# Kernel tuning notes

Hardware: AMD Instinct MI355X
Metric: run time of the kernel (lower is better)

The kernel has to match this reference:

```python
import jax, jax.numpy as jnp
import numpy as np

B, Q, K, C, H, DH, OUT = 32, 512, 512, 256, 8, 32, 256


def setup_inputs() -> dict:
    key = jax.random.key(0)
    ks = jax.random.split(key, 11)
    s = 1.0 / np.sqrt(C)
    return {
        "q_data": jax.random.normal(ks[0], (B, Q, C), jnp.float32),
        "m_data": jax.random.normal(ks[1], (B, K, C), jnp.float32),
        "bias": jax.random.normal(ks[2], (B, 1, Q, K), jnp.float32),
        "nonbatched_bias": jax.random.normal(ks[3], (H, Q, K), jnp.float32),
        "query_w": jax.random.normal(ks[4], (C, H, DH), jnp.float32) * s,
        "key_w": jax.random.normal(ks[5], (C, H, DH), jnp.float32) * s,
        "value_w": jax.random.normal(ks[6], (C, H, DH), jnp.float32) * s,
        "gating_w": jax.random.normal(ks[7], (C, H, DH), jnp.float32) * s,
        "gating_b": jax.random.normal(ks[8], (H, DH), jnp.float32),
        "output_w": jax.random.normal(ks[9], (H, DH, OUT), jnp.float32) * (1.0 / np.sqrt(H * DH)),
        "output_b": jax.random.normal(ks[10], (OUT,), jnp.float32),
    }


def reference(q_data, m_data, bias, nonbatched_bias, query_w, key_w, value_w,
              gating_w, gating_b, output_w, output_b):
    key_dim = query_w.shape[-1]  # per-head key dim
    q = jnp.einsum('bqa,ahc->bqhc', q_data, query_w) * key_dim ** (-0.5)
    k = jnp.einsum('bka,ahc->bkhc', m_data, key_w)
    v = jnp.einsum('bka,ahc->bkhc', m_data, value_w)
    logits = jnp.einsum('bqhc,bkhc->bhqk', q, k) + bias  # [B,H,Q,K]
    logits = logits + nonbatched_bias[None]  # broadcast over batch
    logits = jnp.clip(logits, -1e8, 1e8)
    weights = jax.nn.softmax(logits, axis=-1)
    weighted_avg = jnp.einsum('bhqk,bkhc->bqhc', weights, v)
    gate = jax.nn.sigmoid(jnp.einsum('bqc,chv->bqhv', q_data, gating_w) + gating_b)
    weighted_avg = weighted_avg * gate
    return jnp.einsum('bqhc,hco->bqo', weighted_avg, output_w) + output_b
```

## Files before the change

kernel.cpp:

```cpp
#include <hip/hip_runtime.h>

typedef unsigned short u16;
typedef __attribute__((ext_vector_type(4))) short short4v;
typedef __attribute__((ext_vector_type(8))) short bf16x8;
typedef __attribute__((ext_vector_type(4))) float f32x4;

union Pack8 { u16 h[8]; int4 v; bf16x8 b; };
union Frag8 { bf16x8 v8; short4v h4[2]; };

__device__ __forceinline__ f32x4 mfma16(bf16x8 a, bf16x8 b, f32x4 c) {
    return __builtin_amdgcn_mfma_f32_16x16x32_bf16(a, b, c, 0, 0, 0);
}

__device__ __forceinline__ float bf2f(u16 u) {
    unsigned int x = ((unsigned int)u) << 16;
    return __builtin_bit_cast(float, x);
}

__device__ __forceinline__ u16 f2bf(float f) {
    unsigned int u = __builtin_bit_cast(unsigned int, f);
    u += 0x7FFF + ((u >> 16) & 1);
    return (u16)(u >> 16);
}

__global__ __launch_bounds__(256) void prep_w2(
    const float* __restrict__ qw, const float* __restrict__ kw,
    const float* __restrict__ vw, const float* __restrict__ gw,
    const float* __restrict__ ow,
    u16* __restrict__ wtq, u16* __restrict__ wtm, u16* __restrict__ wto)
{
    const int which = blockIdx.z;
    const float* s = which == 0 ? qw : which == 1 ? kw : which == 2 ? vw
                   : which == 3 ? gw : ow;
    u16* d; int roff;
    if (which == 0)      { d = wtq; roff = 0; }
    else if (which == 3) { d = wtq; roff = 256; }
    else if (which == 1) { d = wtm; roff = 0; }
    else if (which == 2) { d = wtm; roff = 256; }
    else                 { d = wto; roff = 0; }

    const int n0 = blockIdx.x * 64;
    const int c0 = blockIdx.y * 64;

    __shared__ float T[64][68];
    const int rr = threadIdx.x >> 2;
    const int sg = threadIdx.x & 3;
    #pragma unroll
    for (int j = 0; j < 4; ++j) {
        float4 v = *(const float4*)(&s[(size_t)(c0 + rr) * 256 + n0 + sg * 16 + j * 4]);
        *(float4*)(&T[rr][sg * 16 + j * 4]) = v;
    }
    __syncthreads();
    #pragma unroll
    for (int j = 0; j < 4; ++j) {
        union { u16 h[4]; uint2 v; } p;
        #pragma unroll
        for (int e = 0; e < 4; ++e)
            p.h[e] = f2bf(T[sg * 16 + j * 4 + e][rr]);
        *(uint2*)(&d[(size_t)(roff + n0 + rr) * 256 + c0 + sg * 16 + j * 4]) = p.v;
    }
}

__global__ __launch_bounds__(256) void proj128(
    const float* __restrict__ q_data, const float* __restrict__ m_data,
    const u16* __restrict__ wtq, const u16* __restrict__ wtm,
    const float* __restrict__ gating_b,
    u16* __restrict__ qbuf, u16* __restrict__ kbuf,
    u16* __restrict__ vbuf, u16* __restrict__ gbuf)
{
    const int src = blockIdx.z;
    const float* X = src ? m_data : q_data;
    const u16* W = src ? wtm : wtq;

    const int m0 = blockIdx.x * 128;
    const int n0 = blockIdx.y * 128;

    __shared__ __align__(16) u16 SMEM[2][128][72];
    #define Xs (SMEM[0])
    #define Ws (SMEM[1])

    const int tid  = threadIdx.x;
    const int wave = tid >> 6;
    const int wm   = wave >> 1, wn = wave & 1;
    const int lane = tid & 63;
    const int l16  = lane & 15;
    const int quad = lane >> 4;

    const f32x4 kZero = {0.f, 0.f, 0.f, 0.f};
    f32x4 acc[4][4];
    #pragma unroll
    for (int i = 0; i < 4; ++i)
        #pragma unroll
        for (int j = 0; j < 4; ++j) acc[i][j] = kZero;

    const int r  = tid >> 1;
    const int cs = (tid & 1) * 32;

    for (int k0 = 0; k0 < 256; k0 += 64) {
        __syncthreads();
        #pragma unroll
        for (int i = 0; i < 4; ++i) {
            const float4* xp = (const float4*)(&X[(size_t)(m0 + r) * 256 + k0 + cs + i * 8]);
            float4 xa = xp[0], xb = xp[1];
            Pack8 pk;
            pk.h[0] = f2bf(xa.x); pk.h[1] = f2bf(xa.y);
            pk.h[2] = f2bf(xa.z); pk.h[3] = f2bf(xa.w);
            pk.h[4] = f2bf(xb.x); pk.h[5] = f2bf(xb.y);
            pk.h[6] = f2bf(xb.z); pk.h[7] = f2bf(xb.w);
            *(int4*)(&Xs[r][cs + i * 8]) = pk.v;
            *(int4*)(&Ws[r][cs + i * 8]) = *(const int4*)(&W[(size_t)(n0 + r) * 256 + k0 + cs + i * 8]);
        }
        __syncthreads();
        #pragma unroll
        for (int ks = 0; ks < 2; ++ks) {
            bf16x8 a[4], bb[4];
            #pragma unroll
            for (int mf = 0; mf < 4; ++mf)
                a[mf] = *(const bf16x8*)(&Xs[wm * 64 + mf * 16 + l16][ks * 32 + quad * 8]);
            #pragma unroll
            for (int nf = 0; nf < 4; ++nf)
                bb[nf] = *(const bf16x8*)(&Ws[wn * 64 + nf * 16 + l16][ks * 32 + quad * 8]);
            #pragma unroll
            for (int mf = 0; mf < 4; ++mf)
                #pragma unroll
                for (int nf = 0; nf < 4; ++nf)
                    acc[mf][nf] = mfma16(a[mf], bb[nf], acc[mf][nf]);
        }
    }

    const bool second = (n0 >= 256);
    const int b = m0 >> 9, qi0 = m0 & 511;

    __syncthreads();
    u16* T = &SMEM[0][0][0];

    if (src == 1 && second) {
        #pragma unroll
        for (int nf = 0; nf < 4; ++nf) {
            const int nl_ = wn * 64 + nf * 16 + l16;
            #pragma unroll
            for (int mf = 0; mf < 4; ++mf)
                #pragma unroll
                for (int rr = 0; rr < 4; ++rr) {
                    const int ml = wm * 64 + mf * 16 + quad * 4 + rr;
                    T[nl_ * 136 + ml] = f2bf(acc[mf][nf][rr]);
                }
        }
        __syncthreads();
        const int row = tid >> 1, half = tid & 1;
        const int nl = (n0 - 256) + row;
        const int h = nl >> 5, c = nl & 31;
        u16* dst = &vbuf[((size_t)(b * 8 + h) * 32 + c) * 512 + qi0 + half * 64];
        #pragma unroll
        for (int i = 0; i < 8; ++i)
            *(int4*)(&dst[i * 8]) = *(const int4*)(&T[row * 136 + half * 64 + i * 8]);
        return;
    }

    #pragma unroll
    for (int nf = 0; nf < 4; ++nf) {
        const int nl_ = wn * 64 + nf * 16 + l16;
        const int ng = n0 + nl_;
        #pragma unroll
        for (int mf = 0; mf < 4; ++mf) {
            #pragma unroll
            for (int rr = 0; rr < 4; ++rr) {
                const int ml = wm * 64 + mf * 16 + quad * 4 + rr;
                float v = acc[mf][nf][rr];
                u16 val;
                if (src == 0 && !second) {
                    val = f2bf(v * 0.17677669529663689f);
                } else if (src == 0) {
                    val = f2bf(1.0f / (1.0f + __expf(-(v + gating_b[ng - 256]))));
                } else {
                    val = f2bf(v);
                }
                T[ml * 136 + nl_] = val;
            }
        }
    }
    __syncthreads();

    if (src == 0 && second) {
        const int ml = tid >> 1, sub = tid & 1;
        u16* dst = &gbuf[(size_t)(m0 + ml) * 256 + (n0 - 256) + sub * 64];
        #pragma unroll
        for (int i = 0; i < 8; ++i)
            *(int4*)(&dst[i * 8]) = *(const int4*)(&T[ml * 136 + sub * 64 + i * 8]);
    } else {
        u16* D = (src == 0) ? qbuf : kbuf;
        const int hl = tid & 3, h0 = n0 >> 5;
        #pragma unroll
        for (int p = 0; p < 2; ++p) {
            const int ml = p * 64 + (tid >> 2);
            u16* dst = &D[((size_t)(b * 8 + h0 + hl) * 512 + qi0 + ml) * 32];
            #pragma unroll
            for (int i = 0; i < 4; ++i)
                *(int4*)(&dst[i * 8]) = *(const int4*)(&T[ml * 136 + hl * 32 + i * 8]);
        }
    }
    #undef Xs
    #undef Ws
}

__global__ __launch_bounds__(256) void attn_kernel(
    const u16* __restrict__ qbuf, const u16* __restrict__ kbuf,
    const u16* __restrict__ vbuf, const float* __restrict__ bias,
    const float* __restrict__ nb, const u16* __restrict__ gbuf,
    u16* __restrict__ waG)
{
    const int b = blockIdx.z, h = blockIdx.y, q0 = blockIdx.x * 64;
    const int tid  = threadIdx.x;
    const int wave = tid >> 6;
    const int lane = tid & 63;
    const int l16  = lane & 15;
    const int quad = lane >> 4;

    __shared__ __align__(16) u16   Ks[64][40];
    __shared__ __align__(16) u16   Vs[32][72];
    __shared__ __align__(16) float Bs[4][16][68];

    const int qrow_base = q0 + wave * 16;
    bf16x8 aQ = *(const bf16x8*)(&qbuf[((b * 8 + h) * 512 + qrow_base + l16) * 32 + quad * 8]);

    const f32x4 kZero = {0.f, 0.f, 0.f, 0.f};
    f32x4 oacc[2] = {kZero, kZero};
    float lsum = 0.f;

    const int krow = tid >> 2, kseg = tid & 3;
    const int vr = tid >> 3,  vseg = tid & 7;
    const int br = lane >> 2, bc = (lane & 3) * 16;
    const u16* kbase = &kbuf[(size_t)(b * 8 + h) * 512 * 32];
    const u16* vbase = &vbuf[(size_t)(b * 8 + h) * 32 * 512];
    const float* bl = &bias[((size_t)b * 512 + qrow_base + br) * 512];
    const float* nl = &nb[((size_t)h * 512 + qrow_base + br) * 512];

    int4 kreg = *(const int4*)(&kbase[krow * 32 + kseg * 8]);
    int4 vreg = *(const int4*)(&vbase[vr * 512 + vseg * 8]);
    float4 bbp[4], nnp[4];
    #pragma unroll
    for (int i = 0; i < 4; ++i) {
        bbp[i] = *(const float4*)(&bl[bc + i * 4]);
        nnp[i] = *(const float4*)(&nl[bc + i * 4]);
    }

    for (int kt = 0; kt < 8; ++kt) {
        __syncthreads();
        *(int4*)(&Ks[krow][kseg * 8]) = kreg;
        *(int4*)(&Vs[vr][vseg * 8])   = vreg;
        #pragma unroll
        for (int i = 0; i < 4; ++i) {
            float4 s = make_float4(bbp[i].x + nnp[i].x, bbp[i].y + nnp[i].y,
                                   bbp[i].z + nnp[i].z, bbp[i].w + nnp[i].w);
            *(float4*)(&Bs[wave][br][bc + i * 4]) = s;
        }
        __syncthreads();

        if (kt < 7) {
            const int kk1 = (kt + 1) * 64;
            kreg = *(const int4*)(&kbase[(kk1 + krow) * 32 + kseg * 8]);
            vreg = *(const int4*)(&vbase[vr * 512 + kk1 + vseg * 8]);
            #pragma unroll
            for (int i = 0; i < 4; ++i) {
                bbp[i] = *(const float4*)(&bl[kk1 + bc + i * 4]);
                nnp[i] = *(const float4*)(&nl[kk1 + bc + i * 4]);
            }
        }

        float p[4][4];
        #pragma unroll
        for (int kn = 0; kn < 4; ++kn) {
            f32x4 cb = *(const f32x4*)(&Bs[wave][l16][kn * 16 + quad * 4]);
            bf16x8 aK = *(const bf16x8*)(&Ks[kn * 16 + l16][quad * 8]);
            f32x4 st = mfma16(aK, aQ, cb);
            #pragma unroll
            for (int rr = 0; rr < 4; ++rr) {
                float pv = __expf(st[rr]);
                p[kn][rr] = pv;
                lsum += pv;
            }
        }

        #pragma unroll
        for (int pr = 0; pr < 2; ++pr) {
            Frag8 bP;
            #pragma unroll
            for (int rr = 0; rr < 4; ++rr) {
                bP.h4[0][rr] = (short)f2bf(p[2 * pr][rr]);
                bP.h4[1][rr] = (short)f2bf(p[2 * pr + 1][rr]);
            }
            #pragma unroll
            for (int ct = 0; ct < 2; ++ct) {
                Frag8 aV;
                aV.h4[0] = *(const short4v*)(&Vs[ct * 16 + l16][pr * 32 + quad * 4]);
                aV.h4[1] = *(const short4v*)(&Vs[ct * 16 + l16][pr * 32 + 16 + quad * 4]);
                oacc[ct] = mfma16(aV.v8, bP.v8, oacc[ct]);
            }
        }
    }

    lsum += __shfl_xor(lsum, 16, 64);
    lsum += __shfl_xor(lsum, 32, 64);
    const float linv = 1.0f / lsum;

    u16* OsW = (u16*)&Bs[wave][0][0];
    #pragma unroll
    for (int ct = 0; ct < 2; ++ct)
        #pragma unroll
        for (int rr = 0; rr < 4; ++rr)
            OsW[l16 * 40 + ct * 16 + quad * 4 + rr] = f2bf(oacc[ct][rr] * linv);

    __asm__ __volatile__("" ::: "memory");

    const int orow = lane >> 2, osg = lane & 3;
    Pack8 ov, gv;
    ov.v = *(const int4*)(&OsW[orow * 40 + osg * 8]);
    size_t gidx = ((size_t)(b * 512 + q0 + wave * 16 + orow)) * 256 + h * 32 + osg * 8;
    gv.v = *(const int4*)(&gbuf[gidx]);
    Pack8 outv;
    #pragma unroll
    for (int i = 0; i < 8; ++i)
        outv.h[i] = f2bf(bf2f(ov.h[i]) * bf2f(gv.h[i]));
    *(int4*)(&waG[gidx]) = outv.v;
}

__global__ __launch_bounds__(256) void out_gemm128(
    const u16* __restrict__ waG, const u16* __restrict__ wto,
    const float* __restrict__ out_b, float* __restrict__ out)
{
    const int m0 = blockIdx.x * 128;
    const int n0 = blockIdx.y * 128;

    __shared__ __align__(16) u16 Xs[128][72];
    __shared__ __align__(16) u16 Ws[128][72];

    const int tid  = threadIdx.x;
    const int wave = tid >> 6;
    const int wm   = wave >> 1, wn = wave & 1;
    const int lane = tid & 63;
    const int l16  = lane & 15;
    const int quad = lane >> 4;

    const f32x4 kZero = {0.f, 0.f, 0.f, 0.f};
    f32x4 acc[4][4];
    #pragma unroll
    for (int i = 0; i < 4; ++i)
        #pragma unroll
        for (int j = 0; j < 4; ++j) acc[i][j] = kZero;

    const int r  = tid >> 1;
    const int cs = (tid & 1) * 32;

    for (int k0 = 0; k0 < 256; k0 += 64) {
        __syncthreads();
        #pragma unroll
        for (int i = 0; i < 4; ++i) {
            *(int4*)(&Xs[r][cs + i * 8]) = *(const int4*)(&waG[(size_t)(m0 + r) * 256 + k0 + cs + i * 8]);
            *(int4*)(&Ws[r][cs + i * 8]) = *(const int4*)(&wto[(size_t)(n0 + r) * 256 + k0 + cs + i * 8]);
        }
        __syncthreads();
        #pragma unroll
        for (int ks = 0; ks < 2; ++ks) {
            bf16x8 a[4], bb[4];
            #pragma unroll
            for (int mf = 0; mf < 4; ++mf)
                a[mf] = *(const bf16x8*)(&Xs[wm * 64 + mf * 16 + l16][ks * 32 + quad * 8]);
            #pragma unroll
            for (int nf = 0; nf < 4; ++nf)
                bb[nf] = *(const bf16x8*)(&Ws[wn * 64 + nf * 16 + l16][ks * 32 + quad * 8]);
            #pragma unroll
            for (int mf = 0; mf < 4; ++mf)
                #pragma unroll
                for (int nf = 0; nf < 4; ++nf)
                    acc[mf][nf] = mfma16(a[mf], bb[nf], acc[mf][nf]);
        }
    }

    #pragma unroll
    for (int nf = 0; nf < 4; ++nf) {
        const int n = n0 + wn * 64 + nf * 16 + l16;
        const float ob = out_b[n];
        #pragma unroll
        for (int mf = 0; mf < 4; ++mf) {
            #pragma unroll
            for (int rr = 0; rr < 4; ++rr) {
                const int m = m0 + wm * 64 + mf * 16 + quad * 4 + rr;
                out[(size_t)m * 256 + n] = acc[mf][nf][rr] + ob;
            }
        }
    }
}

extern "C" void kernel_launch(void* const* d_in, const int* in_sizes, int n_in,
                              void* d_out, int out_size, void* d_ws, size_t ws_size,
                              hipStream_t stream)
{
    const float* q_data = (const float*)d_in[0];
    const float* m_data = (const float*)d_in[1];
    const float* bias   = (const float*)d_in[2];
    const float* nb     = (const float*)d_in[3];
    const float* qw     = (const float*)d_in[4];
    const float* kw     = (const float*)d_in[5];
    const float* vw     = (const float*)d_in[6];
    const float* gw     = (const float*)d_in[7];
    const float* gb     = (const float*)d_in[8];
    const float* ow     = (const float*)d_in[9];
    const float* ob     = (const float*)d_in[10];

    char* ws = (char*)d_ws;
    u16* wtq  = (u16*)ws;
    u16* wtm  = wtq + 131072;
    u16* wto  = wtm + 131072;
    u16* qbuf = wto + 65536;
    u16* kbuf = qbuf + 4194304;
    u16* vbuf = kbuf + 4194304;
    u16* gbuf = vbuf + 4194304;
    u16* waG  = gbuf + 4194304;

    prep_w2<<<dim3(4, 4, 5), 256, 0, stream>>>(qw, kw, vw, gw, ow, wtq, wtm, wto);
    proj128<<<dim3(128, 4, 2), 256, 0, stream>>>(q_data, m_data, wtq, wtm, gb,
                                                 qbuf, kbuf, vbuf, gbuf);
    attn_kernel<<<dim3(8, 8, 32), 256, 0, stream>>>(qbuf, kbuf, vbuf, bias, nb,
                                                    gbuf, waG);
    out_gemm128<<<dim3(128, 2), 256, 0, stream>>>(waG, wto, ob, (float*)d_out);
}
```

Before: 218.6 us.

## Double-buffer K/V tiles in LDS and use one barrier per iteration

Splits the shared K and V tiles into two ping-pong buffers. The next tile is stored to LDS while the current one is consumed, and global loads are prefetched two tiles ahead. This removes one of the two __syncthreads per key tile and hides more global latency. The cost is doubled K/V LDS footprint and more live registers, which may lower occupancy.

```diff
diff --git a/kernel.cpp b/kernel.cpp
--- a/kernel.cpp
+++ b/kernel.cpp
@@ -216,8 +216,8 @@
     const int l16  = lane & 15;
     const int quad = lane >> 4;
 
-    __shared__ __align__(16) u16   Ks[64][40];
-    __shared__ __align__(16) u16   Vs[32][72];
+    __shared__ __align__(16) u16   Ks[2][64][40];
+    __shared__ __align__(16) u16   Vs[2][32][72];
     __shared__ __align__(16) float Bs[4][16][68];
 
     const int qrow_base = q0 + wave * 16;
@@ -243,36 +243,57 @@
         bbp[i] = *(const float4*)(&bl[bc + i * 4]);
         nnp[i] = *(const float4*)(&nl[bc + i * 4]);
     }
+    *(int4*)(&Ks[0][krow][kseg * 8]) = kreg;
+    *(int4*)(&Vs[0][vr][vseg * 8])   = vreg;
+    #pragma unroll
+    for (int i = 0; i < 4; ++i) {
+        float4 s = make_float4(bbp[i].x + nnp[i].x, bbp[i].y + nnp[i].y,
+                               bbp[i].z + nnp[i].z, bbp[i].w + nnp[i].w);
+        *(float4*)(&Bs[wave][br][bc + i * 4]) = s;
+    }
+    kreg = *(const int4*)(&kbase[(64 + krow) * 32 + kseg * 8]);
+    vreg = *(const int4*)(&vbase[vr * 512 + 64 + vseg * 8]);
+    #pragma unroll
+    for (int i = 0; i < 4; ++i) {
+        bbp[i] = *(const float4*)(&bl[64 + bc + i * 4]);
+        nnp[i] = *(const float4*)(&nl[64 + bc + i * 4]);
+    }
+    __syncthreads();
 
     for (int kt = 0; kt < 8; ++kt) {
-        __syncthreads();
-        *(int4*)(&Ks[krow][kseg * 8]) = kreg;
-        *(int4*)(&Vs[vr][vseg * 8])   = vreg;
-        #pragma unroll
-        for (int i = 0; i < 4; ++i) {
-            float4 s = make_float4(bbp[i].x + nnp[i].x, bbp[i].y + nnp[i].y,
-                                   bbp[i].z + nnp[i].z, bbp[i].w + nnp[i].w);
-            *(float4*)(&Bs[wave][br][bc + i * 4]) = s;
-        }
-        __syncthreads();
-
+        const int buf = kt & 1;
         if (kt < 7) {
-            const int kk1 = (kt + 1) * 64;
-            kreg = *(const int4*)(&kbase[(kk1 + krow) * 32 + kseg * 8]);
-            vreg = *(const int4*)(&vbase[vr * 512 + kk1 + vseg * 8]);
+            *(int4*)(&Ks[buf ^ 1][krow][kseg * 8]) = kreg;
+            *(int4*)(&Vs[buf ^ 1][vr][vseg * 8])   = vreg;
+        }
+        f32x4 cb[4];
+        #pragma unroll
+        for (int kn = 0; kn < 4; ++kn)
+            cb[kn] = *(const f32x4*)(&Bs[wave][l16][kn * 16 + quad * 4]);
+        if (kt < 7) {
             #pragma unroll
             for (int i = 0; i < 4; ++i) {
-                bbp[i] = *(const float4*)(&bl[kk1 + bc + i * 4]);
-                nnp[i] = *(const float4*)(&nl[kk1 + bc + i * 4]);
+                float4 s = make_float4(bbp[i].x + nnp[i].x, bbp[i].y + nnp[i].y,
+                                       bbp[i].z + nnp[i].z, bbp[i].w + nnp[i].w);
+                *(float4*)(&Bs[wave][br][bc + i * 4]) = s;
+            }
+        }
+        if (kt < 6) {
+            const int kk2 = (kt + 2) * 64;
+            kreg = *(const int4*)(&kbase[(kk2 + krow) * 32 + kseg * 8]);
+            vreg = *(const int4*)(&vbase[vr * 512 + kk2 + vseg * 8]);
+            #pragma unroll
+            for (int i = 0; i < 4; ++i) {
+                bbp[i] = *(const float4*)(&bl[kk2 + bc + i * 4]);
+                nnp[i] = *(const float4*)(&nl[kk2 + bc + i * 4]);
             }
         }
 
         float p[4][4];
         #pragma unroll
         for (int kn = 0; kn < 4; ++kn) {
-            f32x4 cb = *(const f32x4*)(&Bs[wave][l16][kn * 16 + quad * 4]);
-            bf16x8 aK = *(const bf16x8*)(&Ks[kn * 16 + l16][quad * 8]);
-            f32x4 st = mfma16(aK, aQ, cb);
+            bf16x8 aK = *(const bf16x8*)(&Ks[buf][kn * 16 + l16][quad * 8]);
+            f32x4 st = mfma16(aK, aQ, cb[kn]);
             #pragma unroll
             for (int rr = 0; rr < 4; ++rr) {
                 float pv = __expf(st[rr]);
@@ -292,11 +313,12 @@
             #pragma unroll
             for (int ct = 0; ct < 2; ++ct) {
                 Frag8 aV;
-                aV.h4[0] = *(const short4v*)(&Vs[ct * 16 + l16][pr * 32 + quad * 4]);
-                aV.h4[1] = *(const short4v*)(&Vs[ct * 16 + l16][pr * 32 + 16 + quad * 4]);
+                aV.h4[0] = *(const short4v*)(&Vs[buf][ct * 16 + l16][pr * 32 + quad * 4]);
+                aV.h4[1] = *(const short4v*)(&Vs[buf][ct * 16 + l16][pr * 32 + 16 + quad * 4]);
                 oacc[ct] = mfma16(aV.v8, bP.v8, oacc[ct]);
             }
         }
+        __syncthreads();
     }
 
     lsum += __shfl_xor(lsum, 16, 64);
```

After: 212.8 us. -2.7%, faster.
